# Kernel tuning notes

Hardware: AMD Instinct MI355X
Metric: run time of the kernel (lower is better)

## Reference

```python
import jax, jax.numpy as jnp
import numpy as np

N_NODES = 8192
K = 32

def setup_inputs() -> dict:
    key = jax.random.key(0)
    kA, kI = jax.random.split(key)
    A = jax.random.normal(kA, (N_NODES, N_NODES), dtype=jnp.float32)
    idx = jnp.arange(N_NODES, dtype=jnp.int64)  # unused by forward, kept for signature fidelity
    return {"A": A, "idx": idx}

def reference(A, idx):
    # adj = relu(A)
    adj = jax.nn.relu(A)
    # row-wise top-k indices, scatter 1.0 into a zero mask, multiply
    _, indices = jax.lax.top_k(adj, K)            # [N, K]
    rows = jnp.arange(adj.shape[0])[:, None]      # [N, 1]
    mask = jnp.zeros_like(adj).at[rows, indices].set(1.0)
    return adj * mask
```

## Files before the change

kernel.cpp:

```cpp
#include <hip/hip_runtime.h>


constexpr int N     = 8192;
constexpr int K     = 32;
constexpr int HB    = 1024;
constexpr int CAP   = 512;
constexpr int SLOTS = CAP / 64;
constexpr int BB    = 128;
constexpr int BLOCK = 256;
constexpr int PSLOT = 4;
constexpr float TSPEC = 2.0f;

typedef float f4 __attribute__((ext_vector_type(4)));

__device__ __forceinline__ bool find_cutoff16(const unsigned* hist, int lane,
                                              int& B, int& G) {
    unsigned s = 0;
    #pragma unroll
    for (int i = 0; i < 16; ++i)
        s += hist[lane * 16 + ((i + lane) & 15)];
    unsigned acc = s;
    #pragma unroll
    for (int off = 1; off < 64; off <<= 1) {
        unsigned t = __shfl_down(acc, off, 64);
        if (lane + off < 64) acc += t;
    }
    unsigned long long m = __ballot(acc >= (unsigned)K);
    if (m == 0ull) return false;
    int g = 63 - __clzll((long long)m);
    unsigned above = (g < 63) ? (unsigned)__shfl((int)acc, g + 1, 64) : 0u;
    unsigned h  = (lane < 16) ? hist[g * 16 + lane] : 0u;
    unsigned a2 = h;
    #pragma unroll
    for (int off = 1; off < 64; off <<= 1) {
        unsigned t = __shfl_down(a2, off, 64);
        if (lane + off < 64) a2 += t;
    }
    unsigned long long m2 = __ballot(above + a2 >= (unsigned)K);
    int bl = 63 - __clzll((long long)m2);
    B = g * 16 + bl;
    G = (int)(above + (unsigned)__shfl((int)a2, bl, 64)
                    - (unsigned)__shfl((int)h,  bl, 64));
    return true;
}

struct Patches {
    float pval[PSLOT][BLOCK];
    int   pcol[PSLOT][BLOCK];
};
union USpace {
    unsigned hist[HB];
    Patches  p;
};

__global__ __launch_bounds__(BLOCK)
void topk_relu_kernel(const float* __restrict__ A, float* __restrict__ Out) {
    const int row  = blockIdx.x;
    const int tid  = threadIdx.x;
    const int lane = tid & 63;
    const int wave = tid >> 6;

    __shared__ USpace   u;
    __shared__ float    cv[CAP];
    __shared__ int      cc[CAP];
    __shared__ float    bbv[BB];
    __shared__ int      bbc[BB];
    __shared__ unsigned pcnt[BLOCK];
    __shared__ unsigned ccnt;
    __shared__ int      fb;

    #pragma unroll
    for (int i = 0; i < HB / BLOCK; ++i) u.hist[tid + i * BLOCK] = 0u;
    pcnt[tid] = 0u;
    if (tid == 0) { ccnt = 0u; fb = 0; }
    __syncthreads();

    const f4* __restrict__ Arow = reinterpret_cast<const f4*>(A + (size_t)row * N);
    #pragma unroll
    for (int i = 0; i < 8; ++i) {
        f4 v = Arow[i * BLOCK + tid];
        #pragma unroll
        for (int c = 0; c < 4; ++c) {
            float f = v[c];
            if (f > TSPEC) {
                atomicAdd(&u.hist[(__float_as_uint(f) >> 20) - 1024], 1u);
                unsigned ix = atomicAdd(&ccnt, 1u);
                if (ix < CAP) { cv[ix] = f; cc[ix] = (i * BLOCK + tid) * 4 + c; }
            }
        }
    }
    __syncthreads();

    f4* __restrict__ Orow4 = reinterpret_cast<f4*>(Out + (size_t)row * N);

    if (wave == 0) {
        int B, G;
        bool ok = find_cutoff16(u.hist, lane, B, G);
        const unsigned Call = ccnt;
        if (!ok || Call > (unsigned)CAP) {
            fb = 1;
        } else {
            const int R = K - G;
            const int C = (int)Call;
            int total = 0;
            #pragma unroll
            for (int s = 0; s < SLOTS; ++s) {
                const int j = lane + s * 64;
                bool flag = false; float fv = 0.0f; int fc = 0;
                if (j < C) {
                    fv = cv[j];
                    if ((int)((__float_as_uint(fv) >> 20) - 1024) == B) {
                        flag = true; fc = cc[j];
                    }
                }
                unsigned long long m = __ballot(flag);
                if (flag) {
                    int pos = total + __popcll(m & ((1ull << lane) - 1ull));
                    if (pos < BB) { bbv[pos] = fv; bbc[pos] = fc; }
                }
                total += (int)__popcll(m);
            }
            if (total > BB) {
                fb = 1;
            } else {
                const int T = total;
                float mv0 = -1.0f, mv1 = -1.0f; int mc0 = 0x7fffffff, mc1 = 0x7fffffff;
                if (lane      < T) { mv0 = bbv[lane];      mc0 = bbc[lane]; }
                if (lane + 64 < T) { mv1 = bbv[lane + 64]; mc1 = bbc[lane + 64]; }
                int r0 = 0, r1 = 0;
                for (int j = 0; j < T; ++j) {
                    const float vj = bbv[j];
                    const int   cj = bbc[j];
                    if (vj > mv0 || (vj == mv0 && cj < mc0)) r0++;
                    if (vj > mv1 || (vj == mv1 && cj < mc1)) r1++;
                }
                float bv = 0.0f; int bc = -1; bool found = false;
                if (lane      < T && r0 == R - 1) { bv = mv0; bc = mc0; found = true; }
                if (lane + 64 < T && r1 == R - 1) { bv = mv1; bc = mc1; found = true; }
                float vR = __int_as_float(0x7f800000);
                int   cR = -1;
                unsigned long long bm = __ballot(found);
                if (bm != 0ull) {
                    int src = (int)__ffsll((long long)bm) - 1;
                    vR = __shfl(bv, src, 64);
                    cR = __shfl(bc, src, 64);
                }
                #pragma unroll
                for (int s = 0; s < SLOTS; ++s) {
                    const int j = lane + s * 64;
                    if (j < C) {
                        float fv = cv[j]; int fc = cc[j];
                        if (fv > vR || (fv == vR && fc <= cR)) {
                            int owner = (fc >> 2) & (BLOCK - 1);
                            unsigned p = atomicAdd(&pcnt[owner], 1u);
                            if (p < (unsigned)PSLOT) {
                                u.p.pval[p][owner] = fv;
                                u.p.pcol[p][owner] = fc;
                            } else {
                                fb = 1;
                            }
                        }
                    }
                }
            }
        }
    }
    __syncthreads();

    if (!fb) {
        const unsigned cnt = pcnt[tid];
        const float v0 = u.p.pval[0][tid], v1 = u.p.pval[1][tid],
                    v2 = u.p.pval[2][tid], v3 = u.p.pval[3][tid];
        const int   c0 = u.p.pcol[0][tid], c1 = u.p.pcol[1][tid],
                    c2 = u.p.pcol[2][tid], c3 = u.p.pcol[3][tid];
        unsigned m8 = 0;
        if (cnt > 0) m8 |= 1u << (c0 >> 10);
        if (cnt > 1) m8 |= 1u << (c1 >> 10);
        if (cnt > 2) m8 |= 1u << (c2 >> 10);
        if (cnt > 3) m8 |= 1u << (c3 >> 10);
        #pragma unroll
        for (int i = 0; i < 8; ++i) {
            f4 w = {0.0f, 0.0f, 0.0f, 0.0f};
            if (m8 & (1u << i)) {
                #define APPLY(CC, VV, KI)                                          \
                    if (cnt > (KI) && ((CC) >> 10) == i) {                         \
                        const int cm = (CC) & 3;                                   \
                        w[0] = (cm == 0) ? (VV) : w[0];                            \
                        w[1] = (cm == 1) ? (VV) : w[1];                            \
                        w[2] = (cm == 2) ? (VV) : w[2];                            \
                        w[3] = (cm == 3) ? (VV) : w[3];                            \
                    }
                APPLY(c0, v0, 0) APPLY(c1, v1, 1) APPLY(c2, v2, 2) APPLY(c3, v3, 3)
                #undef APPLY
            }
            __builtin_nontemporal_store(w, Orow4 + i * BLOCK + tid);
        }
        return;
    }

    #pragma unroll
    for (int i = 0; i < HB / BLOCK; ++i) u.hist[tid + i * BLOCK] = 0u;
    if (tid == 0) ccnt = 0u;
    __syncthreads();
    #pragma unroll
    for (int i = 0; i < 8; ++i) {
        f4 v = Arow[i * BLOCK + tid];
        #pragma unroll
        for (int c = 0; c < 4; ++c) {
            float f = v[c];
            if (f > 0.0f) atomicAdd(&u.hist[__float_as_uint(f) >> 21], 1u);
        }
    }
    __syncthreads();
    int B, G;
    if (!find_cutoff16(u.hist, lane, B, G)) { B = -1; G = 0; }
    if (B >= 0) {
        #pragma unroll
        for (int i = 0; i < 8; ++i) {
            f4 v = Arow[i * BLOCK + tid];
            #pragma unroll
            for (int c = 0; c < 4; ++c) {
                float f = v[c];
                if (f > 0.0f && (int)(__float_as_uint(f) >> 21) == B) {
                    unsigned ix = atomicAdd(&ccnt, 1u);
                    if (ix < CAP) { cv[ix] = f; cc[ix] = (i * BLOCK + tid) * 4 + c; }
                }
            }
        }
    }
    __syncthreads();

    float vR = 0.0f;
    int   cR = -1;
    if (B >= 0) {
        const int R = K - G;
        const int C = (int)min(ccnt, (unsigned)CAP);
        float mv[SLOTS]; int mc[SLOTS]; int rk[SLOTS];
        #pragma unroll
        for (int s = 0; s < SLOTS; ++s) {
            const int j = lane + s * 64;
            if (j < C) { mv[s] = cv[j]; mc[s] = cc[j]; }
            else       { mv[s] = -1.0f; mc[s] = 0x7fffffff; }
            rk[s] = 0;
        }
        for (int j = 0; j < C; ++j) {
            const float vj = cv[j];
            const int   cj = cc[j];
            #pragma unroll
            for (int s = 0; s < SLOTS; ++s)
                if (vj > mv[s] || (vj == mv[s] && cj < mc[s])) rk[s]++;
        }
        float bv = 0.0f; int bc = -1; bool found = false;
        #pragma unroll
        for (int s = 0; s < SLOTS; ++s)
            if (lane + s * 64 < C && rk[s] == R - 1) { bv = mv[s]; bc = mc[s]; found = true; }
        vR = __int_as_float(0x7f800000);
        unsigned long long bm = __ballot(found);
        if (bm != 0ull) {
            int src = (int)__ffsll((long long)bm) - 1;
            vR = __shfl(bv, src, 64);
            cR = __shfl(bc, src, 64);
        }
    }

    #pragma unroll
    for (int i = 0; i < 8; ++i) {
        f4 v = Arow[i * BLOCK + tid];
        f4 w;
        #pragma unroll
        for (int c = 0; c < 4; ++c) {
            float f   = v[c];
            int   col = (i * BLOCK + tid) * 4 + c;
            w[c] = ((f > vR) || (f == vR && col <= cR)) ? f : 0.0f;
        }
        __builtin_nontemporal_store(w, Orow4 + i * BLOCK + tid);
    }
}

extern "C" void kernel_launch(void* const* d_in, const int* in_sizes, int n_in,
                              void* d_out, int out_size, void* d_ws, size_t ws_size,
                              hipStream_t stream) {
    const float* A   = (const float*)d_in[0];
    float*       Out = (float*)d_out;
    (void)in_sizes; (void)n_in; (void)d_ws; (void)ws_size; (void)out_size;
    topk_relu_kernel<<<dim3(N), dim3(BLOCK), 0, stream>>>(A, Out);
}
```

Measured before the change: 91.89 us.

## Split into select-and-zero kernel plus patch kernel to overlap zero stores

```diff
diff --git a/kernel.cpp b/kernel.cpp
--- a/kernel.cpp
+++ b/kernel.cpp
@@ -13,6 +13,12 @@
 
 typedef float f4 __attribute__((ext_vector_type(4)));
 
+__device__ __forceinline__ void lgkm_barrier() {
+    asm volatile("s_waitcnt lgkmcnt(0)" ::: "memory");
+    __builtin_amdgcn_s_barrier();
+    asm volatile("" ::: "memory");
+}
+
 __device__ __forceinline__ bool find_cutoff16(const unsigned* hist, int lane,
                                               int& B, int& G) {
     unsigned s = 0;
@@ -44,36 +50,26 @@
     return true;
 }
 
-struct Patches {
-    float pval[PSLOT][BLOCK];
-    int   pcol[PSLOT][BLOCK];
-};
-union USpace {
-    unsigned hist[HB];
-    Patches  p;
-};
-
 __global__ __launch_bounds__(BLOCK)
-void topk_relu_kernel(const float* __restrict__ A, float* __restrict__ Out) {
+void select_zero_kernel(const float* __restrict__ A, float* __restrict__ Out,
+                        int* __restrict__ flags) {
     const int row  = blockIdx.x;
     const int tid  = threadIdx.x;
     const int lane = tid & 63;
     const int wave = tid >> 6;
 
-    __shared__ USpace   u;
+    __shared__ unsigned hist[HB];
     __shared__ float    cv[CAP];
     __shared__ int      cc[CAP];
     __shared__ float    bbv[BB];
     __shared__ int      bbc[BB];
-    __shared__ unsigned pcnt[BLOCK];
     __shared__ unsigned ccnt;
     __shared__ int      fb;
 
     #pragma unroll
-    for (int i = 0; i < HB / BLOCK; ++i) u.hist[tid + i * BLOCK] = 0u;
-    pcnt[tid] = 0u;
+    for (int i = 0; i < HB / BLOCK; ++i) hist[tid + i * BLOCK] = 0u;
     if (tid == 0) { ccnt = 0u; fb = 0; }
-    __syncthreads();
+    lgkm_barrier();
 
     const f4* __restrict__ Arow = reinterpret_cast<const f4*>(A + (size_t)row * N);
     #pragma unroll
@@ -83,24 +79,35 @@
         for (int c = 0; c < 4; ++c) {
             float f = v[c];
             if (f > TSPEC) {
-                atomicAdd(&u.hist[(__float_as_uint(f) >> 20) - 1024], 1u);
+                atomicAdd(&hist[(__float_as_uint(f) >> 20) - 1024], 1u);
                 unsigned ix = atomicAdd(&ccnt, 1u);
                 if (ix < CAP) { cv[ix] = f; cc[ix] = (i * BLOCK + tid) * 4 + c; }
             }
         }
     }
-    __syncthreads();
-
+
+    __builtin_amdgcn_sched_barrier(0);
     f4* __restrict__ Orow4 = reinterpret_cast<f4*>(Out + (size_t)row * N);
+    const f4 z = {0.0f, 0.0f, 0.0f, 0.0f};
+    #pragma unroll
+    for (int i = 0; i < 8; ++i) {
+        const int q = i * BLOCK + tid;
+        if (q >= 16)
+            __builtin_nontemporal_store(z, Orow4 + q);
+    }
+
+    lgkm_barrier();
 
     if (wave == 0) {
         int B, G;
-        bool ok = find_cutoff16(u.hist, lane, B, G);
+        bool ok = find_cutoff16(hist, lane, B, G);
         const unsigned Call = ccnt;
-        if (!ok || Call > (unsigned)CAP) {
-            fb = 1;
-        } else {
-            const int R = K - G;
+        bool bad = (!ok) || (Call > (unsigned)CAP);
+        float vR = __int_as_float(0x7f800000);
+        int   cR = -1;
+        int   R  = 0;
+        if (!bad) {
+            R = K - G;
             const int C = (int)Call;
             int total = 0;
             #pragma unroll
@@ -121,7 +128,7 @@
                 total += (int)__popcll(m);
             }
             if (total > BB) {
-                fb = 1;
+                bad = true;
             } else {
                 const int T = total;
                 float mv0 = -1.0f, mv1 = -1.0f; int mc0 = 0x7fffffff, mc1 = 0x7fffffff;
@@ -137,13 +144,222 @@
                 float bv = 0.0f; int bc = -1; bool found = false;
                 if (lane      < T && r0 == R - 1) { bv = mv0; bc = mc0; found = true; }
                 if (lane + 64 < T && r1 == R - 1) { bv = mv1; bc = mc1; found = true; }
-                float vR = __int_as_float(0x7f800000);
-                int   cR = -1;
                 unsigned long long bm = __ballot(found);
                 if (bm != 0ull) {
                     int src = (int)__ffsll((long long)bm) - 1;
                     vR = __shfl(bv, src, 64);
                     cR = __shfl(bc, src, 64);
+                }
+            }
+        }
+        if (bad) {
+            if (lane == 0) fb = 1;
+        } else {
+            const int C = (int)Call;
+            float2* __restrict__ Op2 = reinterpret_cast<float2*>(Out + (size_t)row * N);
+            int nsel = 0;
+            #pragma unroll
+            for (int s = 0; s < SLOTS; ++s) {
+                const int j = lane + s * 64;
+                bool flag = false; float fv = 0.0f; int fc = 0;
+                if (j < C) {
+                    fv = cv[j]; fc = cc[j];
+                    flag = (fv > vR) || (fv == vR && fc <= cR);
+                }
+                unsigned long long m = __ballot(flag);
+                if (flag) {
+                    int pos = nsel + __popcll(m & ((1ull << lane) - 1ull));
+                    if (pos < K) {
+                        float2 p; p.x = fv; p.y = __int_as_float(fc);
+                        Op2[pos] = p;
+                    }
+                }
+                nsel += (int)__popcll(m);
+            }
+            if (lane == 0) flags[row] = 0;
+        }
+    }
+    lgkm_barrier();
+    if (!fb) return;
+
+    asm volatile("s_waitcnt vmcnt(0)" ::: "memory");
+    if (tid == 0) { flags[row] = 1; ccnt = 0u; }
+    #pragma unroll
+    for (int i = 0; i < HB / BLOCK; ++i) hist[tid + i * BLOCK] = 0u;
+    __syncthreads();
+    #pragma unroll
+    for (int i = 0; i < 8; ++i) {
+        f4 v = Arow[i * BLOCK + tid];
+        #pragma unroll
+        for (int c = 0; c < 4; ++c) {
+            float f = v[c];
+            if (f > 0.0f) atomicAdd(&hist[__float_as_uint(f) >> 21], 1u);
+        }
+    }
+    __syncthreads();
+    int B, G;
+    if (!find_cutoff16(hist, lane, B, G)) { B = -1; G = 0; }
+    if (B >= 0) {
+        #pragma unroll
+        for (int i = 0; i < 8; ++i) {
+            f4 v = Arow[i * BLOCK + tid];
+            #pragma unroll
+            for (int c = 0; c < 4; ++c) {
+                float f = v[c];
+                if (f > 0.0f && (int)(__float_as_uint(f) >> 21) == B) {
+                    unsigned ix = atomicAdd(&ccnt, 1u);
+                    if (ix < CAP) { cv[ix] = f; cc[ix] = (i * BLOCK + tid) * 4 + c; }
+                }
+            }
+        }
+    }
+    __syncthreads();
+
+    float vR = 0.0f;
+    int   cR = -1;
+    if (B >= 0) {
+        const int R = K - G;
+        const int C = (int)min(ccnt, (unsigned)CAP);
+        float mv[SLOTS]; int mc[SLOTS]; int rk[SLOTS];
+        #pragma unroll
+        for (int s = 0; s < SLOTS; ++s) {
+            const int j = lane + s * 64;
+            if (j < C) { mv[s] = cv[j]; mc[s] = cc[j]; }
+            else       { mv[s] = -1.0f; mc[s] = 0x7fffffff; }
+            rk[s] = 0;
+        }
+        for (int j = 0; j < C; ++j) {
+            const float vj = cv[j];
+            const int   cj = cc[j];
+            #pragma unroll
+            for (int s = 0; s < SLOTS; ++s)
+                if (vj > mv[s] || (vj == mv[s] && cj < mc[s])) rk[s]++;
+        }
+        float bv = 0.0f; int bc = -1; bool found = false;
+        #pragma unroll
+        for (int s = 0; s < SLOTS; ++s)
+            if (lane + s * 64 < C && rk[s] == R - 1) { bv = mv[s]; bc = mc[s]; found = true; }
+        vR = __int_as_float(0x7f800000);
+        unsigned long long bm = __ballot(found);
+        if (bm != 0ull) {
+            int src = (int)__ffsll((long long)bm) - 1;
+            vR = __shfl(bv, src, 64);
+            cR = __shfl(bc, src, 64);
+        }
+    }
+    #pragma unroll
+    for (int i = 0; i < 8; ++i) {
+        f4 v = Arow[i * BLOCK + tid];
+        f4 w;
+        #pragma unroll
+        for (int c = 0; c < 4; ++c) {
+            float f   = v[c];
+            int   col = (i * BLOCK + tid) * 4 + c;
+            w[c] = ((f > vR) || (f == vR && col <= cR)) ? f : 0.0f;
+        }
+        __builtin_nontemporal_store(w, Orow4 + i * BLOCK + tid);
+    }
+}
+
+__global__ __launch_bounds__(BLOCK)
+void patch_kernel(float* __restrict__ Out, const int* __restrict__ flags) {
+    const int row  = (blockIdx.x * BLOCK + threadIdx.x) >> 6;
+    const int lane = threadIdx.x & 63;
+    if (flags[row]) return;
+    float* __restrict__ Orow = Out + (size_t)row * N;
+    float val = 0.0f; int col = 0;
+    if (lane < K) {
+        float2 p = reinterpret_cast<const float2*>(Orow)[lane];
+        val = p.x; col = __float_as_int(p.y);
+    }
+    asm volatile("s_waitcnt vmcnt(0)" ::: "memory");
+    Orow[lane] = 0.0f;
+    asm volatile("s_waitcnt vmcnt(0)" ::: "memory");
+    if (lane < K) Orow[col] = val;
+}
+
+struct Patches { float pval[PSLOT][BLOCK]; int pcol[PSLOT][BLOCK]; };
+union USpace { unsigned hist[HB]; Patches p; };
+
+__global__ __launch_bounds__(BLOCK)
+void topk_relu_single(const float* __restrict__ A, float* __restrict__ Out) {
+    const int row  = blockIdx.x;
+    const int tid  = threadIdx.x;
+    const int lane = tid & 63;
+    const int wave = tid >> 6;
+    __shared__ USpace   u;
+    __shared__ float    cv[CAP];
+    __shared__ int      cc[CAP];
+    __shared__ float    bbv[BB];
+    __shared__ int      bbc[BB];
+    __shared__ unsigned pcnt[BLOCK];
+    __shared__ unsigned ccnt;
+    __shared__ int      fb;
+    #pragma unroll
+    for (int i = 0; i < HB / BLOCK; ++i) u.hist[tid + i * BLOCK] = 0u;
+    pcnt[tid] = 0u;
+    if (tid == 0) { ccnt = 0u; fb = 0; }
+    __syncthreads();
+    const f4* __restrict__ Arow = reinterpret_cast<const f4*>(A + (size_t)row * N);
+    #pragma unroll
+    for (int i = 0; i < 8; ++i) {
+        f4 v = Arow[i * BLOCK + tid];
+        #pragma unroll
+        for (int c = 0; c < 4; ++c) {
+            float f = v[c];
+            if (f > TSPEC) {
+                atomicAdd(&u.hist[(__float_as_uint(f) >> 20) - 1024], 1u);
+                unsigned ix = atomicAdd(&ccnt, 1u);
+                if (ix < CAP) { cv[ix] = f; cc[ix] = (i * BLOCK + tid) * 4 + c; }
+            }
+        }
+    }
+    __syncthreads();
+    f4* __restrict__ Orow4 = reinterpret_cast<f4*>(Out + (size_t)row * N);
+    if (wave == 0) {
+        int B, G;
+        bool ok = find_cutoff16(u.hist, lane, B, G);
+        const unsigned Call = ccnt;
+        if (!ok || Call > (unsigned)CAP) { fb = 1; }
+        else {
+            const int R = K - G;
+            const int C = (int)Call;
+            int total = 0;
+            #pragma unroll
+            for (int s = 0; s < SLOTS; ++s) {
+                const int j = lane + s * 64;
+                bool flag = false; float fv = 0.0f; int fc = 0;
+                if (j < C) {
+                    fv = cv[j];
+                    if ((int)((__float_as_uint(fv) >> 20) - 1024) == B) { flag = true; fc = cc[j]; }
+                }
+                unsigned long long m = __ballot(flag);
+                if (flag) {
+                    int pos = total + __popcll(m & ((1ull << lane) - 1ull));
+                    if (pos < BB) { bbv[pos] = fv; bbc[pos] = fc; }
+                }
+                total += (int)__popcll(m);
+            }
+            if (total > BB) { fb = 1; }
+            else {
+                const int T = total;
+                float mv0 = -1.0f, mv1 = -1.0f; int mc0 = 0x7fffffff, mc1 = 0x7fffffff;
+                if (lane      < T) { mv0 = bbv[lane];      mc0 = bbc[lane]; }
+                if (lane + 64 < T) { mv1 = bbv[lane + 64]; mc1 = bbc[lane + 64]; }
+                int r0 = 0, r1 = 0;
+                for (int j = 0; j < T; ++j) {
+                    const float vj = bbv[j]; const int cj = bbc[j];
+                    if (vj > mv0 || (vj == mv0 && cj < mc0)) r0++;
+                    if (vj > mv1 || (vj == mv1 && cj < mc1)) r1++;
+                }
+                float bv = 0.0f; int bc = -1; bool found = false;
+                if (lane      < T && r0 == R - 1) { bv = mv0; bc = mc0; found = true; }
+                if (lane + 64 < T && r1 == R - 1) { bv = mv1; bc = mc1; found = true; }
+                float vR = __int_as_float(0x7f800000); int cR = -1;
+                unsigned long long bm = __ballot(found);
+                if (bm != 0ull) {
+                    int src = (int)__ffsll((long long)bm) - 1;
+                    vR = __shfl(bv, src, 64); cR = __shfl(bc, src, 64);
                 }
                 #pragma unroll
                 for (int s = 0; s < SLOTS; ++s) {
@@ -153,12 +369,8 @@
                         if (fv > vR || (fv == vR && fc <= cR)) {
                             int owner = (fc >> 2) & (BLOCK - 1);
                             unsigned p = atomicAdd(&pcnt[owner], 1u);
-                            if (p < (unsigned)PSLOT) {
-                                u.p.pval[p][owner] = fv;
-                                u.p.pcol[p][owner] = fc;
-                            } else {
-                                fb = 1;
-                            }
+                            if (p < (unsigned)PSLOT) { u.p.pval[p][owner] = fv; u.p.pcol[p][owner] = fc; }
+                            else fb = 1;
                         }
                     }
                 }
@@ -166,7 +378,6 @@
         }
     }
     __syncthreads();
-
     if (!fb) {
         const unsigned cnt = pcnt[tid];
         const float v0 = u.p.pval[0][tid], v1 = u.p.pval[1][tid],
@@ -197,7 +408,6 @@
         }
         return;
     }
-
     #pragma unroll
     for (int i = 0; i < HB / BLOCK; ++i) u.hist[tid + i * BLOCK] = 0u;
     if (tid == 0) ccnt = 0u;
@@ -229,9 +439,7 @@
         }
     }
     __syncthreads();
-
-    float vR = 0.0f;
-    int   cR = -1;
+    float vR = 0.0f; int cR = -1;
     if (B >= 0) {
         const int R = K - G;
         const int C = (int)min(ccnt, (unsigned)CAP);
@@ -244,8 +452,7 @@
             rk[s] = 0;
         }
         for (int j = 0; j < C; ++j) {
-            const float vj = cv[j];
-            const int   cj = cc[j];
+            const float vj = cv[j]; const int cj = cc[j];
             #pragma unroll
             for (int s = 0; s < SLOTS; ++s)
                 if (vj > mv[s] || (vj == mv[s] && cj < mc[s])) rk[s]++;
@@ -258,19 +465,16 @@
         unsigned long long bm = __ballot(found);
         if (bm != 0ull) {
             int src = (int)__ffsll((long long)bm) - 1;
-            vR = __shfl(bv, src, 64);
-            cR = __shfl(bc, src, 64);
-        }
-    }
-
+            vR = __shfl(bv, src, 64); cR = __shfl(bc, src, 64);
+        }
+    }
     #pragma unroll
     for (int i = 0; i < 8; ++i) {
         f4 v = Arow[i * BLOCK + tid];
         f4 w;
         #pragma unroll
         for (int c = 0; c < 4; ++c) {
-            float f   = v[c];
-            int   col = (i * BLOCK + tid) * 4 + c;
+            float f = v[c]; int col = (i * BLOCK + tid) * 4 + c;
             w[c] = ((f > vR) || (f == vR && col <= cR)) ? f : 0.0f;
         }
         __builtin_nontemporal_store(w, Orow4 + i * BLOCK + tid);
@@ -282,6 +486,12 @@
                               hipStream_t stream) {
     const float* A   = (const float*)d_in[0];
     float*       Out = (float*)d_out;
-    (void)in_sizes; (void)n_in; (void)d_ws; (void)ws_size; (void)out_size;
-    topk_relu_kernel<<<dim3(N), dim3(BLOCK), 0, stream>>>(A, Out);
-}
+    (void)in_sizes; (void)n_in; (void)out_size;
+    if (ws_size >= (size_t)N * sizeof(int)) {
+        int* flags = (int*)d_ws;
+        select_zero_kernel<<<dim3(N), dim3(BLOCK), 0, stream>>>(A, Out, flags);
+        patch_kernel<<<dim3(N / 4), dim3(BLOCK), 0, stream>>>(Out, flags);
+    } else {
+        topk_relu_single<<<dim3(N), dim3(BLOCK), 0, stream>>>(A, Out);
+    }
+}
```

Measured after the change: 115.1 us. +25.3%, slower.
